# Performance work log

Hardware: AMD Instinct MI355X
Metric: run time of the kernel (lower is better)

Reference implementation:

```python
import jax, jax.numpy as jnp
import numpy as np

N_NODES = 50000
N_EDGES = 800000
D_IN = 128
D_OUT = 64


def setup_inputs() -> dict:
    key = jax.random.key(0)
    k1, k2, k3, k4 = jax.random.split(key, 4)
    x = jax.random.normal(k1, (N_NODES, D_IN), dtype=jnp.float32)
    W = jax.random.normal(k2, (D_OUT, D_IN), dtype=jnp.float32) * (1.0 / np.sqrt(D_IN))
    b = jnp.zeros((D_OUT,), dtype=jnp.float32)
    row = jax.random.randint(k3, (N_EDGES,), 0, N_NODES, dtype=jnp.int32)
    col = jax.random.randint(k4, (N_EDGES,), 0, N_NODES, dtype=jnp.int32)
    return {"x": x, "W": W, "b": b, "row": row, "col": col}


def reference(x, W, b, row, col):
    # Linear projection: [N, D_in] -> [N, D_out]
    h = x @ W.T + b
    n = x.shape[0]
    # Row-normalized SpMM: out[i] = (1/deg(i)) * sum_{(i,j) in E} h[j]
    msg = h[col]  # gather source features: [E, D_out]
    summed = jax.ops.segment_sum(msg, row, num_segments=n)
    deg = jax.ops.segment_sum(jnp.ones_like(row, dtype=h.dtype), row, num_segments=n)
    out = summed / jnp.maximum(deg, 1.0)[:, None]
    return out
```

## Files before the change

### kernel.cpp

```cpp
#include <hip/hip_runtime.h>
#include <hip/hip_bf16.h>

#define D_IN   128
#define D_OUT  64
#define CAP    64
#define MAX_USHORT_NODES 65536
#define BIN_SHIFT 8
#define MAX_BINS  256
#define BIN_CAP   8192
#define P1_BLOCKS 256
#define P1_THREADS 512
#define P2_THREADS 512

using frag_ab = __attribute__((ext_vector_type(8))) short;
using frag_cd = __attribute__((ext_vector_type(4))) float;

static __device__ __forceinline__ short f2bf(float f) {
    union { float f; unsigned u; } v; v.f = f;
    unsigned r = v.u + 0x7FFFu + ((v.u >> 16) & 1u);
    return (short)(r >> 16);
}
static __device__ __forceinline__ float bflo(unsigned w) {
    union { unsigned u; float f; } v; v.u = w << 16; return v.f;
}
static __device__ __forceinline__ float bfhi(unsigned w) {
    union { unsigned u; float f; } v; v.u = w & 0xFFFF0000u; return v.f;
}

__global__ void proj_kernel(const float* __restrict__ x,
                            const float* __restrict__ W,
                            const float* __restrict__ bvec,
                            unsigned short* __restrict__ h,
                            int n_nodes) {
    const int lane = (int)threadIdx.x & 63;
    const int wid  = (int)((blockIdx.x * blockDim.x + threadIdx.x) >> 6);
    const int nwaves = (int)((gridDim.x * blockDim.x) >> 6);
    const int m    = lane & 15;
    const int quad = lane >> 4;

    frag_ab Bf[4][4];
#pragma unroll
    for (int kk = 0; kk < 4; ++kk) {
#pragma unroll
        for (int nt = 0; nt < 4; ++nt) {
            const float* wp = W + (size_t)(nt * 16 + m) * D_IN + kk * 32 + quad * 8;
            const float4 w0 = *(const float4*)wp;
            const float4 w1 = *(const float4*)(wp + 4);
            frag_ab f;
            f[0] = f2bf(w0.x); f[1] = f2bf(w0.y); f[2] = f2bf(w0.z); f[3] = f2bf(w0.w);
            f[4] = f2bf(w1.x); f[5] = f2bf(w1.y); f[6] = f2bf(w1.z); f[7] = f2bf(w1.w);
            Bf[kk][nt] = f;
        }
    }
    float bb[4];
#pragma unroll
    for (int nt = 0; nt < 4; ++nt) bb[nt] = bvec[nt * 16 + m];

    const int ntiles = (n_nodes + 15) / 16;
    for (int tile = wid; tile < ntiles; tile += nwaves) {
        const int node_base = tile * 16;
        int arow = node_base + m;
        if (arow > n_nodes - 1) arow = n_nodes - 1;

        float4 xv[8];
        const float* xr = x + (size_t)arow * D_IN + quad * 8;
#pragma unroll
        for (int kk = 0; kk < 4; ++kk) {
            xv[2 * kk]     = *(const float4*)(xr + kk * 32);
            xv[2 * kk + 1] = *(const float4*)(xr + kk * 32 + 4);
        }

        frag_cd acc[4];
#pragma unroll
        for (int nt = 0; nt < 4; ++nt) {
            acc[nt][0] = bb[nt]; acc[nt][1] = bb[nt];
            acc[nt][2] = bb[nt]; acc[nt][3] = bb[nt];
        }
#pragma unroll
        for (int kk = 0; kk < 4; ++kk) {
            const float4 x0 = xv[2 * kk], x1 = xv[2 * kk + 1];
            frag_ab A;
            A[0] = f2bf(x0.x); A[1] = f2bf(x0.y); A[2] = f2bf(x0.z); A[3] = f2bf(x0.w);
            A[4] = f2bf(x1.x); A[5] = f2bf(x1.y); A[6] = f2bf(x1.z); A[7] = f2bf(x1.w);
#pragma unroll
            for (int nt = 0; nt < 4; ++nt)
                acc[nt] = __builtin_amdgcn_mfma_f32_16x16x32_bf16(A, Bf[kk][nt],
                                                                  acc[nt], 0, 0, 0);
        }
#pragma unroll
        for (int nt = 0; nt < 4; ++nt) {
#pragma unroll
            for (int r = 0; r < 4; ++r) {
                const int node = node_base + quad * 4 + r;
                if (node < n_nodes)
                    h[(size_t)node * D_OUT + nt * 16 + m] =
                        (unsigned short)f2bf(acc[nt][r]);
            }
        }
    }
}

__global__ __launch_bounds__(P1_THREADS)
void binpass1_kernel(const int* __restrict__ row, const int* __restrict__ col,
                     unsigned* __restrict__ scratch, int* __restrict__ cursor,
                     int* __restrict__ ovfA_cnt, unsigned* __restrict__ ovfA_list,
                     int ovfA_cap, int n_edges, int n_bins) {
    __shared__ int hist[MAX_BINS];
    __shared__ int base[MAX_BINS];
    const int per = (n_edges + P1_BLOCKS - 1) / P1_BLOCKS;
    const int e0 = (int)blockIdx.x * per;
    const int e1 = min(e0 + per, n_edges);

    for (int i = threadIdx.x; i < n_bins; i += P1_THREADS) hist[i] = 0;
    __syncthreads();
    for (int e = e0 + (int)threadIdx.x; e < e1; e += P1_THREADS)
        atomicAdd(&hist[row[e] >> BIN_SHIFT], 1);
    __syncthreads();
    for (int i = threadIdx.x; i < n_bins; i += P1_THREADS) {
        const int hcnt = hist[i];
        base[i] = hcnt > 0 ? atomicAdd(&cursor[i * 16], hcnt) : 0;
        hist[i] = 0;
    }
    __syncthreads();
    for (int e = e0 + (int)threadIdx.x; e < e1; e += P1_THREADS) {
        const int r = row[e];
        const int c = col[e];
        const int bn = r >> BIN_SHIFT;
        const int loc = atomicAdd(&hist[bn], 1);
        const int off = base[bn] + loc;
        if (off < BIN_CAP) {
            scratch[(size_t)bn * BIN_CAP + off] =
                (unsigned)(r & 255) | ((unsigned)c << 8);
        } else {
            const int k = atomicAdd(ovfA_cnt, 1);
            if (k < ovfA_cap) ovfA_list[k] = (unsigned)r | ((unsigned)c << 16);
        }
    }
}

__global__ __launch_bounds__(P2_THREADS)
void binpass2_kernel(const unsigned* __restrict__ scratch,
                     const int* __restrict__ cursor,
                     int* __restrict__ deg, unsigned short* __restrict__ bucket,
                     int* __restrict__ ovfB_cnt, unsigned* __restrict__ ovfB_list,
                     int ovfB_cap, int n_nodes) {
    __shared__ int ldeg[256];
    __shared__ unsigned short lbuck[256 * CAP];
    const int bin = (int)blockIdx.x;
    const int node0 = bin << BIN_SHIFT;
    const int nrows = min(256, n_nodes - node0);
    int cnt = cursor[bin * 16]; if (cnt > BIN_CAP) cnt = BIN_CAP;

    for (int i = threadIdx.x; i < 256; i += P2_THREADS) ldeg[i] = 0;
    __syncthreads();
    for (int i = threadIdx.x; i < cnt; i += P2_THREADS) {
        const unsigned rec = scratch[(size_t)bin * BIN_CAP + i];
        const int rl = rec & 255;
        const int c  = (int)(rec >> 8);
        const int s = atomicAdd(&ldeg[rl], 1);
        if (s < CAP) {
            lbuck[(rl << 6) + s] = (unsigned short)c;
        } else {
            const int k = atomicAdd(ovfB_cnt, 1);
            if (k < ovfB_cap)
                ovfB_list[k] = (unsigned)(node0 + rl) | ((unsigned)c << 16);
        }
    }
    __syncthreads();
    for (int i = threadIdx.x; i < nrows; i += P2_THREADS) deg[node0 + i] = ldeg[i];
    uint4* dst = (uint4*)(bucket + (size_t)node0 * CAP);
    const uint4* src = (const uint4*)lbuck;
    const int nu4 = nrows * 8;
    for (int i = threadIdx.x; i < nu4; i += P2_THREADS) dst[i] = src[i];
}

__global__ void degfix_kernel(const unsigned* __restrict__ ovfA_list,
                              const int* __restrict__ ovfA_cnt, int ovfA_cap,
                              int* __restrict__ deg) {
    int cnt = *ovfA_cnt; if (cnt > ovfA_cap) cnt = ovfA_cap;
    for (int t = (int)(blockIdx.x * blockDim.x + threadIdx.x); t < cnt;
         t += (int)(gridDim.x * blockDim.x))
        atomicAdd(&deg[ovfA_list[t] & 0xFFFFu], 1);
}

__global__ void gather_kernel(const uint2* __restrict__ h64,
                              const int* __restrict__ deg,
                              const unsigned short* __restrict__ bucket,
                              float4* __restrict__ out4,
                              int n_nodes) {
    const int lane = (int)threadIdx.x & 63;
    const int q = lane >> 4;
    const int j = lane & 15;
    const int wave = (int)((blockIdx.x * blockDim.x + threadIdx.x) >> 6);
    const int nwaves = (int)((gridDim.x * blockDim.x) >> 6);

    int node = wave;
    if (node >= n_nodes) return;
    int d_nxt = deg[node];
    int my_nxt = (int)bucket[(size_t)node * CAP + lane];

    while (node < n_nodes) {
        const int d = d_nxt;
        const int mycol = my_nxt;
        const int nxt = node + nwaves;
        if (nxt < n_nodes) {
            d_nxt = deg[nxt];
            my_nxt = (int)bucket[(size_t)nxt * CAP + lane];
        }

        const int dc = d < CAP ? d : CAP;
        const int ngr = (dc + 3) >> 2;
        float a0 = 0.f, a1 = 0.f, a2 = 0.f, a3 = 0.f;
        float b0 = 0.f, b1 = 0.f, b2 = 0.f, b3 = 0.f;
        int g = 0;
        for (; g + 2 <= ngr; g += 2) {
            const int iA = __shfl(mycol, 4 * g + q);
            const int iB = __shfl(mycol, 4 * g + 4 + q);
            uint2 wA = h64[(size_t)iA * 16 + j];
            uint2 wB = h64[(size_t)iB * 16 + j];
            if (4 * g + q >= dc)     { wA.x = 0u; wA.y = 0u; }
            if (4 * g + 4 + q >= dc) { wB.x = 0u; wB.y = 0u; }
            a0 += bflo(wA.x); a1 += bfhi(wA.x); a2 += bflo(wA.y); a3 += bfhi(wA.y);
            b0 += bflo(wB.x); b1 += bfhi(wB.x); b2 += bflo(wB.y); b3 += bfhi(wB.y);
        }
        for (; g < ngr; ++g) {
            const int iA = __shfl(mycol, 4 * g + q);
            uint2 wA = h64[(size_t)iA * 16 + j];
            if (4 * g + q >= dc) { wA.x = 0u; wA.y = 0u; }
            a0 += bflo(wA.x); a1 += bfhi(wA.x); a2 += bflo(wA.y); a3 += bfhi(wA.y);
        }
        a0 += b0; a1 += b1; a2 += b2; a3 += b3;
        a0 += __shfl_xor(a0, 16); a0 += __shfl_xor(a0, 32);
        a1 += __shfl_xor(a1, 16); a1 += __shfl_xor(a1, 32);
        a2 += __shfl_xor(a2, 16); a2 += __shfl_xor(a2, 32);
        a3 += __shfl_xor(a3, 16); a3 += __shfl_xor(a3, 32);
        if (q == 0) {
            const float inv = 1.0f / fmaxf((float)d, 1.0f);
            float4 o;
            o.x = a0 * inv; o.y = a1 * inv; o.z = a2 * inv; o.w = a3 * inv;
            out4[(size_t)node * (D_OUT / 4) + j] = o;
        }
        node = nxt;
    }
}

__global__ void ovf_apply_kernel(const unsigned short* __restrict__ h,
                                 const int* __restrict__ deg,
                                 const unsigned* __restrict__ listA,
                                 const int* __restrict__ cntA_p, int capA,
                                 const unsigned* __restrict__ listB,
                                 const int* __restrict__ cntB_p, int capB,
                                 float* __restrict__ out) {
    int cA = *cntA_p; if (cA > capA) cA = capA;
    int cB = *cntB_p; if (cB > capB) cB = capB;
    const long long n_tasks = (long long)(cA + cB) * D_OUT;
    long long t = (long long)blockIdx.x * blockDim.x + threadIdx.x;
    const long long stride = (long long)gridDim.x * blockDim.x;
    for (; t < n_tasks; t += stride) {
        const int k = (int)(t >> 6);
        const int lane = (int)(t & 63);
        const unsigned rec = (k < cA) ? listA[k] : listB[k - cA];
        const int r = (int)(rec & 0xFFFFu);
        const int c = (int)(rec >> 16);
        union { unsigned u; float f; } v;
        v.u = ((unsigned)h[(size_t)c * D_OUT + lane]) << 16;
        atomicAdd(&out[(size_t)r * D_OUT + lane],
                  v.f / fmaxf((float)deg[r], 1.0f));
    }
}

__global__ void proj_only_kernel(const float* __restrict__ x,
                                 const float* __restrict__ W,
                                 const float* __restrict__ bvec,
                                 float* __restrict__ h, int n_nodes) {
    const int lane = (int)threadIdx.x & 63;
    const int wave = (int)((blockIdx.x * blockDim.x + threadIdx.x) >> 6);
    const int nwaves = (int)((gridDim.x * blockDim.x) >> 6);
    const float bias = bvec[lane];
    for (int node = wave; node < n_nodes; node += nwaves) {
        const float* xr = &x[(size_t)node * D_IN];
        float acc = bias;
#pragma unroll
        for (int k = 0; k < D_IN; ++k) acc += xr[k] * W[lane * D_IN + k];
        h[(size_t)node * D_OUT + lane] = acc;
    }
}

__global__ void scatter_kernel(const float* __restrict__ h,
                               const int* __restrict__ row,
                               const int* __restrict__ col,
                               float* __restrict__ out,
                               int* __restrict__ deg,
                               long long n_tasks) {
    long long t = (long long)blockIdx.x * blockDim.x + threadIdx.x;
    const long long stride = (long long)gridDim.x * blockDim.x;
    for (; t < n_tasks; t += stride) {
        const int e = (int)(t >> 6);
        const int c = (int)(t & 63);
        atomicAdd(&out[(size_t)row[e] * D_OUT + c], h[(size_t)col[e] * D_OUT + c]);
        if (c == 0) atomicAdd(&deg[row[e]], 1);
    }
}

__global__ void div_kernel(float* __restrict__ out,
                           const int* __restrict__ deg, int n_total) {
    int t = blockIdx.x * blockDim.x + threadIdx.x;
    if (t < n_total) {
        out[t] *= 1.0f / fmaxf((float)deg[t >> 6], 1.0f);
    }
}

extern "C" void kernel_launch(void* const* d_in, const int* in_sizes, int n_in,
                              void* d_out, int out_size, void* d_ws, size_t ws_size,
                              hipStream_t stream) {
    const float* x   = (const float*)d_in[0];
    const float* W   = (const float*)d_in[1];
    const float* b   = (const float*)d_in[2];
    const int*   row = (const int*)d_in[3];
    const int*   col = (const int*)d_in[4];
    float* out = (float*)d_out;

    const int n_nodes = in_sizes[0] / D_IN;
    const int n_edges = in_sizes[3];
    const int n_bins  = (n_nodes + 255) >> BIN_SHIFT;

    char* p = (char*)d_ws;
    unsigned short* h = (unsigned short*)p;
    p += (size_t)n_nodes * D_OUT * sizeof(unsigned short);
    int* deg = (int*)p;            p += (size_t)n_nodes * sizeof(int);
    int* ovf_cnts = (int*)p;       p += 256;
    int* cursor = (int*)p;         p += (size_t)MAX_BINS * 16 * sizeof(int);
    unsigned* ovfA_list = (unsigned*)p;  p += (size_t)n_edges * sizeof(unsigned);
    unsigned* ovfB_list = (unsigned*)p;  p += (size_t)n_edges * sizeof(unsigned);
    unsigned short* bucket = (unsigned short*)p;
    p += (size_t)n_nodes * CAP * sizeof(unsigned short);
    unsigned* scratch = (unsigned*)p;
    p += (size_t)n_bins * BIN_CAP * sizeof(unsigned);
    const size_t needed = (size_t)(p - (char*)d_ws);

    if (ws_size >= needed && n_nodes <= MAX_USHORT_NODES) {
        hipMemsetAsync(ovf_cnts, 0, 256 + (size_t)MAX_BINS * 16 * sizeof(int),
                       stream);

        const int ntiles = (n_nodes + 15) / 16;
        const int proj_blocks = (ntiles + 7) / 8;
        proj_kernel<<<proj_blocks, 256, 0, stream>>>(x, W, b, h, n_nodes);

        binpass1_kernel<<<P1_BLOCKS, P1_THREADS, 0, stream>>>(
            row, col, scratch, cursor, &ovf_cnts[0], ovfA_list, n_edges,
            n_edges, n_bins);
        binpass2_kernel<<<n_bins, P2_THREADS, 0, stream>>>(
            scratch, cursor, deg, bucket, &ovf_cnts[1], ovfB_list, n_edges,
            n_nodes);
        degfix_kernel<<<64, 256, 0, stream>>>(ovfA_list, &ovf_cnts[0], n_edges,
                                              deg);

        const int grid = (n_nodes + 3) / 4;
        gather_kernel<<<grid, 256, 0, stream>>>((const uint2*)h, deg, bucket,
                                                (float4*)out, n_nodes);

        ovf_apply_kernel<<<256, 256, 0, stream>>>(h, deg, ovfA_list,
                                                  &ovf_cnts[0], n_edges,
                                                  ovfB_list, &ovf_cnts[1],
                                                  n_edges, out);
    } else {
        float* hf = (float*)d_ws;
        int* degf = (int*)((char*)d_ws + (size_t)n_nodes * D_OUT * sizeof(float));
        hipMemsetAsync(out, 0, (size_t)out_size * sizeof(float), stream);
        hipMemsetAsync(degf, 0, (size_t)n_nodes * sizeof(int), stream);
        proj_only_kernel<<<1024, 256, 0, stream>>>(x, W, b, hf, n_nodes);
        const long long n_tasks = (long long)n_edges * D_OUT;
        scatter_kernel<<<16384, 256, 0, stream>>>(hf, row, col, out, degf, n_tasks);
        const int n_total = n_nodes * D_OUT;
        div_kernel<<<(n_total + 255) / 256, 256, 0, stream>>>(out, degf, n_total);
    }
}
```

Before: 135.1 us.

## Fuse projection with edge binning and fold overflow handling into gather

The projection and first binning pass now run in a single launch, with separate block ranges for each job so the two can overlap. The degree-fix and overflow-apply kernels are gone: binpass2 adds overflow degrees atomically, and the gather kernel scans the overflow lists for its own node. The per-node bucket capacity drops from 64 to 32, which shrinks the bucket writes and reads but pushes more high-degree edges into the overflow lists. Because every node linearly scans both lists, gather cost grows with the overflow count, which is cheap only while those lists stay short.

```diff
diff --git a/kernel.cpp b/kernel.cpp
--- a/kernel.cpp
+++ b/kernel.cpp
@@ -3,13 +3,12 @@
 
 #define D_IN   128
 #define D_OUT  64
-#define CAP    64
+#define CAP    32
 #define MAX_USHORT_NODES 65536
 #define BIN_SHIFT 8
 #define MAX_BINS  256
 #define BIN_CAP   8192
 #define P1_BLOCKS 256
-#define P1_THREADS 512
 #define P2_THREADS 512
 
 using frag_ab = __attribute__((ext_vector_type(8))) short;
@@ -26,15 +25,62 @@
 static __device__ __forceinline__ float bfhi(unsigned w) {
     union { unsigned u; float f; } v; v.u = w & 0xFFFF0000u; return v.f;
 }
-
-__global__ void proj_kernel(const float* __restrict__ x,
+static __device__ __forceinline__ float bf1(unsigned short s) {
+    union { unsigned u; float f; } v; v.u = ((unsigned)s) << 16; return v.f;
+}
+
+__global__ void prep_kernel(const float* __restrict__ x,
                             const float* __restrict__ W,
                             const float* __restrict__ bvec,
                             unsigned short* __restrict__ h,
-                            int n_nodes) {
+                            const int* __restrict__ row,
+                            const int* __restrict__ col,
+                            unsigned* __restrict__ scratch,
+                            int* __restrict__ cursor,
+                            int* __restrict__ ovfA_cnt,
+                            unsigned* __restrict__ ovfA_list,
+                            int ovfA_cap, int n_nodes, int n_edges,
+                            int n_bins, int proj_blocks) {
+    __shared__ int hist[MAX_BINS];
+    __shared__ int base[MAX_BINS];
+
+    if ((int)blockIdx.x >= proj_blocks) {
+        const int bid = (int)blockIdx.x - proj_blocks;
+        const int per = (n_edges + P1_BLOCKS - 1) / P1_BLOCKS;
+        const int e0 = bid * per;
+        const int e1 = min(e0 + per, n_edges);
+
+        for (int i = threadIdx.x; i < n_bins; i += 256) hist[i] = 0;
+        __syncthreads();
+        for (int e = e0 + (int)threadIdx.x; e < e1; e += 256)
+            atomicAdd(&hist[row[e] >> BIN_SHIFT], 1);
+        __syncthreads();
+        for (int i = threadIdx.x; i < n_bins; i += 256) {
+            const int hcnt = hist[i];
+            base[i] = hcnt > 0 ? atomicAdd(&cursor[i * 16], hcnt) : 0;
+            hist[i] = 0;
+        }
+        __syncthreads();
+        for (int e = e0 + (int)threadIdx.x; e < e1; e += 256) {
+            const int r = row[e];
+            const int c = col[e];
+            const int bn = r >> BIN_SHIFT;
+            const int loc = atomicAdd(&hist[bn], 1);
+            const int off = base[bn] + loc;
+            if (off < BIN_CAP) {
+                scratch[(size_t)bn * BIN_CAP + off] =
+                    (unsigned)(r & 255) | ((unsigned)c << 8);
+            } else {
+                const int k = atomicAdd(ovfA_cnt, 1);
+                if (k < ovfA_cap) ovfA_list[k] = (unsigned)r | ((unsigned)c << 16);
+            }
+        }
+        return;
+    }
+
     const int lane = (int)threadIdx.x & 63;
-    const int wid  = (int)((blockIdx.x * blockDim.x + threadIdx.x) >> 6);
-    const int nwaves = (int)((gridDim.x * blockDim.x) >> 6);
+    const int wid  = (int)((blockIdx.x * 256 + threadIdx.x) >> 6);
+    const int nwaves = proj_blocks * 4;
     const int m    = lane & 15;
     const int quad = lane >> 4;
 
@@ -100,56 +146,27 @@
     }
 }
 
-__global__ __launch_bounds__(P1_THREADS)
-void binpass1_kernel(const int* __restrict__ row, const int* __restrict__ col,
-                     unsigned* __restrict__ scratch, int* __restrict__ cursor,
-                     int* __restrict__ ovfA_cnt, unsigned* __restrict__ ovfA_list,
-                     int ovfA_cap, int n_edges, int n_bins) {
-    __shared__ int hist[MAX_BINS];
-    __shared__ int base[MAX_BINS];
-    const int per = (n_edges + P1_BLOCKS - 1) / P1_BLOCKS;
-    const int e0 = (int)blockIdx.x * per;
-    const int e1 = min(e0 + per, n_edges);
-
-    for (int i = threadIdx.x; i < n_bins; i += P1_THREADS) hist[i] = 0;
-    __syncthreads();
-    for (int e = e0 + (int)threadIdx.x; e < e1; e += P1_THREADS)
-        atomicAdd(&hist[row[e] >> BIN_SHIFT], 1);
-    __syncthreads();
-    for (int i = threadIdx.x; i < n_bins; i += P1_THREADS) {
-        const int hcnt = hist[i];
-        base[i] = hcnt > 0 ? atomicAdd(&cursor[i * 16], hcnt) : 0;
-        hist[i] = 0;
-    }
-    __syncthreads();
-    for (int e = e0 + (int)threadIdx.x; e < e1; e += P1_THREADS) {
-        const int r = row[e];
-        const int c = col[e];
-        const int bn = r >> BIN_SHIFT;
-        const int loc = atomicAdd(&hist[bn], 1);
-        const int off = base[bn] + loc;
-        if (off < BIN_CAP) {
-            scratch[(size_t)bn * BIN_CAP + off] =
-                (unsigned)(r & 255) | ((unsigned)c << 8);
-        } else {
-            const int k = atomicAdd(ovfA_cnt, 1);
-            if (k < ovfA_cap) ovfA_list[k] = (unsigned)r | ((unsigned)c << 16);
-        }
-    }
-}
-
 __global__ __launch_bounds__(P2_THREADS)
 void binpass2_kernel(const unsigned* __restrict__ scratch,
                      const int* __restrict__ cursor,
                      int* __restrict__ deg, unsigned short* __restrict__ bucket,
                      int* __restrict__ ovfB_cnt, unsigned* __restrict__ ovfB_list,
-                     int ovfB_cap, int n_nodes) {
+                     int ovfB_cap,
+                     const int* __restrict__ ovfA_cnt,
+                     const unsigned* __restrict__ ovfA_list, int ovfA_cap,
+                     int n_nodes) {
     __shared__ int ldeg[256];
     __shared__ unsigned short lbuck[256 * CAP];
     const int bin = (int)blockIdx.x;
     const int node0 = bin << BIN_SHIFT;
     const int nrows = min(256, n_nodes - node0);
     int cnt = cursor[bin * 16]; if (cnt > BIN_CAP) cnt = BIN_CAP;
+
+    if (bin == 0) {
+        int cA = *ovfA_cnt; if (cA > ovfA_cap) cA = ovfA_cap;
+        for (int k = threadIdx.x; k < cA; k += P2_THREADS)
+            atomicAdd(&deg[ovfA_list[k] & 0xFFFFu], 1);
+    }
 
     for (int i = threadIdx.x; i < 256; i += P2_THREADS) ldeg[i] = 0;
     __syncthreads();
@@ -159,7 +176,7 @@
         const int c  = (int)(rec >> 8);
         const int s = atomicAdd(&ldeg[rl], 1);
         if (s < CAP) {
-            lbuck[(rl << 6) + s] = (unsigned short)c;
+            lbuck[(rl << 5) + s] = (unsigned short)c;
         } else {
             const int k = atomicAdd(ovfB_cnt, 1);
             if (k < ovfB_cap)
@@ -167,25 +184,22 @@
         }
     }
     __syncthreads();
-    for (int i = threadIdx.x; i < nrows; i += P2_THREADS) deg[node0 + i] = ldeg[i];
+    for (int i = threadIdx.x; i < nrows; i += P2_THREADS)
+        atomicAdd(&deg[node0 + i], ldeg[i]);
     uint4* dst = (uint4*)(bucket + (size_t)node0 * CAP);
     const uint4* src = (const uint4*)lbuck;
-    const int nu4 = nrows * 8;
+    const int nu4 = nrows * (CAP / 8);
     for (int i = threadIdx.x; i < nu4; i += P2_THREADS) dst[i] = src[i];
 }
 
-__global__ void degfix_kernel(const unsigned* __restrict__ ovfA_list,
-                              const int* __restrict__ ovfA_cnt, int ovfA_cap,
-                              int* __restrict__ deg) {
-    int cnt = *ovfA_cnt; if (cnt > ovfA_cap) cnt = ovfA_cap;
-    for (int t = (int)(blockIdx.x * blockDim.x + threadIdx.x); t < cnt;
-         t += (int)(gridDim.x * blockDim.x))
-        atomicAdd(&deg[ovfA_list[t] & 0xFFFFu], 1);
-}
-
 __global__ void gather_kernel(const uint2* __restrict__ h64,
+                              const unsigned short* __restrict__ h16,
                               const int* __restrict__ deg,
                               const unsigned short* __restrict__ bucket,
+                              const int* __restrict__ ovf_cnts,
+                              const unsigned* __restrict__ ovfA_list,
+                              const unsigned* __restrict__ ovfB_list,
+                              int ovf_cap,
                               float4* __restrict__ out4,
                               int n_nodes) {
     const int lane = (int)threadIdx.x & 63;
@@ -194,10 +208,13 @@
     const int wave = (int)((blockIdx.x * blockDim.x + threadIdx.x) >> 6);
     const int nwaves = (int)((gridDim.x * blockDim.x) >> 6);
 
+    int cA = ovf_cnts[0]; if (cA > ovf_cap) cA = ovf_cap;
+    int cB = ovf_cnts[1]; if (cB > ovf_cap) cB = ovf_cap;
+
     int node = wave;
     if (node >= n_nodes) return;
     int d_nxt = deg[node];
-    int my_nxt = (int)bucket[(size_t)node * CAP + lane];
+    int my_nxt = (int)bucket[(size_t)node * CAP + (lane & (CAP - 1))];
 
     while (node < n_nodes) {
         const int d = d_nxt;
@@ -205,7 +222,7 @@
         const int nxt = node + nwaves;
         if (nxt < n_nodes) {
             d_nxt = deg[nxt];
-            my_nxt = (int)bucket[(size_t)nxt * CAP + lane];
+            my_nxt = (int)bucket[(size_t)nxt * CAP + (lane & (CAP - 1))];
         }
 
         const int dc = d < CAP ? d : CAP;
@@ -235,37 +252,34 @@
         a2 += __shfl_xor(a2, 16); a2 += __shfl_xor(a2, 32);
         a3 += __shfl_xor(a3, 16); a3 += __shfl_xor(a3, 32);
         if (q == 0) {
+            if (cA + cB > 0) {
+                for (int k = 0; k < cA; ++k) {
+                    const unsigned rec = ovfA_list[k];
+                    if ((int)(rec & 0xFFFFu) == node) {
+                        const int c = (int)(rec >> 16);
+                        a0 += bf1(h16[(size_t)c * D_OUT + 4 * j + 0]);
+                        a1 += bf1(h16[(size_t)c * D_OUT + 4 * j + 1]);
+                        a2 += bf1(h16[(size_t)c * D_OUT + 4 * j + 2]);
+                        a3 += bf1(h16[(size_t)c * D_OUT + 4 * j + 3]);
+                    }
+                }
+                for (int k = 0; k < cB; ++k) {
+                    const unsigned rec = ovfB_list[k];
+                    if ((int)(rec & 0xFFFFu) == node) {
+                        const int c = (int)(rec >> 16);
+                        a0 += bf1(h16[(size_t)c * D_OUT + 4 * j + 0]);
+                        a1 += bf1(h16[(size_t)c * D_OUT + 4 * j + 1]);
+                        a2 += bf1(h16[(size_t)c * D_OUT + 4 * j + 2]);
+                        a3 += bf1(h16[(size_t)c * D_OUT + 4 * j + 3]);
+                    }
+                }
+            }
             const float inv = 1.0f / fmaxf((float)d, 1.0f);
             float4 o;
             o.x = a0 * inv; o.y = a1 * inv; o.z = a2 * inv; o.w = a3 * inv;
             out4[(size_t)node * (D_OUT / 4) + j] = o;
         }
         node = nxt;
-    }
-}
-
-__global__ void ovf_apply_kernel(const unsigned short* __restrict__ h,
-                                 const int* __restrict__ deg,
-                                 const unsigned* __restrict__ listA,
-                                 const int* __restrict__ cntA_p, int capA,
-                                 const unsigned* __restrict__ listB,
-                                 const int* __restrict__ cntB_p, int capB,
-                                 float* __restrict__ out) {
-    int cA = *cntA_p; if (cA > capA) cA = capA;
-    int cB = *cntB_p; if (cB > capB) cB = capB;
-    const long long n_tasks = (long long)(cA + cB) * D_OUT;
-    long long t = (long long)blockIdx.x * blockDim.x + threadIdx.x;
-    const long long stride = (long long)gridDim.x * blockDim.x;
-    for (; t < n_tasks; t += stride) {
-        const int k = (int)(t >> 6);
-        const int lane = (int)(t & 63);
-        const unsigned rec = (k < cA) ? listA[k] : listB[k - cA];
-        const int r = (int)(rec & 0xFFFFu);
-        const int c = (int)(rec >> 16);
-        union { unsigned u; float f; } v;
-        v.u = ((unsigned)h[(size_t)c * D_OUT + lane]) << 16;
-        atomicAdd(&out[(size_t)r * D_OUT + lane],
-                  v.f / fmaxf((float)deg[r], 1.0f));
     }
 }
 
@@ -339,30 +353,24 @@
     const size_t needed = (size_t)(p - (char*)d_ws);
 
     if (ws_size >= needed && n_nodes <= MAX_USHORT_NODES) {
-        hipMemsetAsync(ovf_cnts, 0, 256 + (size_t)MAX_BINS * 16 * sizeof(int),
-                       stream);
+        hipMemsetAsync(deg, 0,
+                       (size_t)n_nodes * sizeof(int) + 256 +
+                       (size_t)MAX_BINS * 16 * sizeof(int), stream);
 
         const int ntiles = (n_nodes + 15) / 16;
-        const int proj_blocks = (ntiles + 7) / 8;
-        proj_kernel<<<proj_blocks, 256, 0, stream>>>(x, W, b, h, n_nodes);
-
-        binpass1_kernel<<<P1_BLOCKS, P1_THREADS, 0, stream>>>(
-            row, col, scratch, cursor, &ovf_cnts[0], ovfA_list, n_edges,
-            n_edges, n_bins);
+        const int proj_blocks = (ntiles + 3) / 4;
+        prep_kernel<<<proj_blocks + P1_BLOCKS, 256, 0, stream>>>(
+            x, W, b, h, row, col, scratch, cursor, &ovf_cnts[0], ovfA_list,
+            n_edges, n_nodes, n_edges, n_bins, proj_blocks);
+
         binpass2_kernel<<<n_bins, P2_THREADS, 0, stream>>>(
             scratch, cursor, deg, bucket, &ovf_cnts[1], ovfB_list, n_edges,
-            n_nodes);
-        degfix_kernel<<<64, 256, 0, stream>>>(ovfA_list, &ovf_cnts[0], n_edges,
-                                              deg);
+            &ovf_cnts[0], ovfA_list, n_edges, n_nodes);
 
         const int grid = (n_nodes + 3) / 4;
-        gather_kernel<<<grid, 256, 0, stream>>>((const uint2*)h, deg, bucket,
-                                                (float4*)out, n_nodes);
-
-        ovf_apply_kernel<<<256, 256, 0, stream>>>(h, deg, ovfA_list,
-                                                  &ovf_cnts[0], n_edges,
-                                                  ovfB_list, &ovf_cnts[1],
-                                                  n_edges, out);
+        gather_kernel<<<grid, 256, 0, stream>>>(
+            (const uint2*)h, h, deg, bucket, ovf_cnts, ovfA_list, ovfB_list,
+            n_edges, (float4*)out, n_nodes);
     } else {
         float* hf = (float*)d_ws;
         int* degf = (int*)((char*)d_ws + (size_t)n_nodes * D_OUT * sizeof(float));
```

New measurement: 136.6 us. Within noise of the previous version (+1.1%).
